# Kernel tuning notes

Hardware: AMD Instinct MI355X
Metric: run time of the kernel (lower is better)

The kernel has to match this reference:

```python
import jax, jax.numpy as jnp
import numpy as np

K, P, Q, D = 16, 1024, 1024, 64  # heads, value-in dim, out dim, head dim; P'=P, Q'=Q, D'=D
B, N = 2, 2048                   # batch, seq (self-attention: M=N)
TEMPERATURE = jnp.sqrt(jnp.float32(D))

def _xavier(key, shape):
    fan_in, fan_out = shape[-2], shape[-1]
    lim = jnp.sqrt(6.0 / (fan_in + fan_out))
    return jax.random.uniform(key, shape, jnp.float32, -lim, lim)

def setup_inputs() -> dict:
    key = jax.random.key(0)
    k0, k1, k2, k3, k4 = jax.random.split(key, 5)
    return {
        'y_prime': jax.random.normal(k0, (B, N, Q), jnp.float32),
        'mask': jnp.zeros((N, N), jnp.float32),  # log-domain additive mask [M,N]
        'Lam_x': _xavier(k1, (K, P, D)),  # Lambda^(x): [K,P',D']
        'Lam_y': _xavier(k2, (K, Q, D)),  # Lambda^(y): [K,Q',D']
        'Th_x': _xavier(k3, (K, P, D)),   # Theta^(x):  [K,P,D]
        'Th_y': _xavier(k4, (K, Q, D)),   # Theta^(y):  [K,Q,D]
    }

def reference(y_prime, mask, Lam_x, Lam_y, Th_x, Th_y):
    # self-attention: x' = x = y'
    x_p = y_prime
    x = x_p
    # key projection: [B,M,K,D']
    r = jnp.einsum('bmp,kpd->bmkd', x_p, Lam_x)
    # bilinear scores: [K,B,M,N]
    r = jnp.einsum('bmkd,kqd,bnq->kbmn', r, Lam_y, y_prime)
    r = r + mask[None, None, :, :]
    # softmax over M (axis=-2), scaled by sqrt(D')
    A = jax.nn.softmax(r / TEMPERATURE, axis=-2)
    # value aggregation: [B,N,K,D]
    r = jnp.einsum('kbmn,bmp,kpd->bnkd', A, x, Th_x)
    # output projection: [B,N,Q]
    return jnp.einsum('bnkd,kqd->bnq', r, Th_y)
```

## Files before the change

kernel.cpp:

```cpp
#include <hip/hip_runtime.h>
#include <hip/hip_bf16.h>

#define KH 16
#define PD 1024
#define QD 1024
#define DD 64
#define BB 2
#define NN 2048
#define BN 4096
#define ST 72
#define SOFT_C 12.0f

typedef unsigned short u16;
typedef __attribute__((ext_vector_type(8))) short bf16x8;
typedef __attribute__((ext_vector_type(4))) short bf16x4;
typedef __attribute__((ext_vector_type(4))) float f32x4;

__device__ __forceinline__ float bf2f(u16 u) {
    return __uint_as_float(((unsigned)u) << 16);
}
__device__ __forceinline__ u16 f2bf(float f) {
    unsigned x = __float_as_uint(f);
    x += 0x7FFFu + ((x >> 16) & 1u);
    return (u16)(x >> 16);
}
__device__ __forceinline__ f32x4 mfma_k32(bf16x8 a, bf16x8 b, f32x4 c) {
    return __builtin_amdgcn_mfma_f32_16x16x32_bf16(a, b, c, 0, 0, 0);
}
__device__ __forceinline__ f32x4 mfma_k16(bf16x4 a, bf16x4 b, f32x4 c) {
#if __has_builtin(__builtin_amdgcn_mfma_f32_16x16x16bf16_1k)
    return __builtin_amdgcn_mfma_f32_16x16x16bf16_1k(a, b, c, 0, 0, 0);
#else
    asm("v_mfma_f32_16x16x16_bf16 %0, %1, %2, %0" : "+v"(c) : "v"(a), "v"(b));
    return c;
#endif
}
__device__ __forceinline__ bf16x8 ldfrag(const u16* base, int r0, int kc, int lane) {
    return *reinterpret_cast<const bf16x8*>(base + (r0 + (lane & 15)) * ST + kc +
                                            ((lane >> 4) << 3));
}
__device__ __forceinline__ bf16x4 ldfrag4(const u16* base, int r0, int kc, int lane) {
    return *reinterpret_cast<const bf16x4*>(base + (r0 + (lane & 15)) * ST + kc +
                                            ((lane >> 4) << 2));
}
__device__ __forceinline__ bf16x8 ldfragL(const u16* base, int r0, int kc, int lane) {
    return *reinterpret_cast<const bf16x8*>(base + ((r0 + (lane & 15)) << 6) + kc +
                                            ((lane >> 4) << 3));
}
__device__ __forceinline__ bf16x4 pack4(float a, float b, float c, float d) {
    union { bf16x4 v; __hip_bfloat162 h[2]; } u;
    u.h[0] = __float22bfloat162_rn(make_float2(a, b));
    u.h[1] = __float22bfloat162_rn(make_float2(c, d));
    return u.v;
}
__device__ __forceinline__ void gl_lds16(const u16* g, u16* l) {
    __builtin_amdgcn_global_load_lds(
        (const __attribute__((address_space(1))) void*)g,
        (__attribute__((address_space(3))) void*)l, 16, 0, 0);
}
template <int ROWS>
__device__ __forceinline__ void stage_dma(const u16* __restrict__ src, int ld,
                                          u16* dst, int lane, int w) {
#pragma unroll
    for (int c = 0; c < ROWS / 32; ++c) {
        int rbase = (w * (ROWS / 32) + c) * 8;
        const u16* g = src + (size_t)(rbase + (lane >> 3)) * ld + ((lane & 7) << 3);
        gl_lds16(g, dst + (rbase << 6));
    }
}
template <int ROWS, int NT>
__device__ __forceinline__ void stage_rows(const u16* __restrict__ src, int ld,
                                           u16* dst, int tid) {
#pragma unroll
    for (int it = 0; it < ROWS * 8 / NT; ++it) {
        int chunk = it * NT + tid;
        int row = chunk >> 3, col = (chunk & 7) << 3;
        *reinterpret_cast<uint4*>(dst + row * ST + col) =
            *reinterpret_cast<const uint4*>(src + row * ld + col);
    }
}

__global__ void detect_kernel(const u16* __restrict__ y, int* flag, int* mnz) {
    __shared__ int cnt;
    if (threadIdx.x == 0) cnt = 0;
    __syncthreads();
    int local = 0;
    for (int i = threadIdx.x; i < 8192; i += 256) {
        u16 u = y[i];
        int e = (u >> 7) & 0xFF;
        if (u == 0 || (e >= 96 && e < 160)) local++;
    }
    atomicAdd(&cnt, local);
    __syncthreads();
    if (threadIdx.x == 0) {
        *flag = (cnt > 7372) ? 1 : 0;
        *mnz = 0;
    }
}

__global__ __launch_bounds__(256) void mcheck_kernel(const void* __restrict__ msrc,
                                                     const int* __restrict__ flag,
                                                     int* mnz) {
    size_t n4 = (size_t)NN * NN / 8;
    if (*flag == 0) n4 *= 2;
    const uint4* p = (const uint4*)msrc;
    unsigned acc = 0;
    for (size_t i = blockIdx.x * 256 + threadIdx.x; i < n4;
         i += (size_t)gridDim.x * 256) {
        uint4 v = p[i];
        acc |= v.x | v.y | v.z | v.w;
    }
    if (acc) atomicOr(mnz, 1);
}

__global__ __launch_bounds__(256) void convert_kernel(
    const void* __restrict__ src, u16* __restrict__ dst, int n,
    const int* __restrict__ flag) {
    int i = (blockIdx.x * 256 + threadIdx.x) * 4;
    if (i >= n) return;
    if (*flag) {
        *reinterpret_cast<uint2*>(dst + i) =
            *reinterpret_cast<const uint2*>((const u16*)src + i);
    } else {
        float4 f = *reinterpret_cast<const float4*>((const float*)src + i);
        u16 t[4] = {f2bf(f.x), f2bf(f.y), f2bf(f.z), f2bf(f.w)};
        *reinterpret_cast<uint2*>(dst + i) = *reinterpret_cast<uint2*>(t);
    }
}

__global__ __launch_bounds__(256) void maskc_kernel(const void* __restrict__ src,
                                                    u16* __restrict__ dst,
                                                    const int* __restrict__ flag,
                                                    const int* __restrict__ mnz) {
    if (*mnz == 0) return;
    size_t i = ((size_t)blockIdx.x * 256 + threadIdx.x) * 8;
    float f[8];
    if (*flag) {
        uint4 v = *reinterpret_cast<const uint4*>((const u16*)src + i);
        u16 t[8];
        *reinterpret_cast<uint4*>(t) = v;
#pragma unroll
        for (int e = 0; e < 8; ++e) f[e] = bf2f(t[e]);
    } else {
        float4 a = *reinterpret_cast<const float4*>((const float*)src + i);
        float4 b = *reinterpret_cast<const float4*>((const float*)src + i + 4);
        f[0] = a.x; f[1] = a.y; f[2] = a.z; f[3] = a.w;
        f[4] = b.x; f[5] = b.y; f[6] = b.z; f[7] = b.w;
    }
    u16 t[8];
#pragma unroll
    for (int e = 0; e < 8; ++e) t[e] = f2bf(f[e] * 0.125f);
    *reinterpret_cast<uint4*>(dst + i) = *reinterpret_cast<uint4*>(t);
}

__global__ __launch_bounds__(256) void prew_kernel(
    const void* __restrict__ s0, const void* __restrict__ s1,
    const void* __restrict__ s2, const void* __restrict__ s3,
    u16* __restrict__ LamXt, u16* __restrict__ LamYt, u16* __restrict__ ThXt,
    u16* __restrict__ ThYr, const int* __restrict__ flag) {
    int z = blockIdx.z, k = blockIdx.y, tid = threadIdx.x;
    int isbf = *flag;
    if (z < 3) {
        const void* src = (z == 0) ? s0 : (z == 1) ? s1 : s2;
        u16* dst = (z == 0) ? LamXt : (z == 1) ? LamYt : ThXt;
        float scale = (z == 1) ? 0.125f : 1.0f;
        int p0 = blockIdx.x * 64;
        __shared__ float T[64][65];
        const u16* s16 = (const u16*)src + ((size_t)k * PD + p0) * DD;
        const float* s32 = (const float*)src + ((size_t)k * PD + p0) * DD;
#pragma unroll
        for (int it = 0; it < 2; ++it) {
            int chunk = it * 256 + tid;
            int row = chunk >> 3, c8 = (chunk & 7) << 3;
            float f[8];
            if (isbf) {
                uint4 v = *reinterpret_cast<const uint4*>(s16 + row * DD + c8);
                u16 t[8];
                *reinterpret_cast<uint4*>(t) = v;
#pragma unroll
                for (int e = 0; e < 8; ++e) f[e] = bf2f(t[e]);
            } else {
                float4 a = *reinterpret_cast<const float4*>(s32 + row * DD + c8);
                float4 b = *reinterpret_cast<const float4*>(s32 + row * DD + c8 + 4);
                f[0] = a.x; f[1] = a.y; f[2] = a.z; f[3] = a.w;
                f[4] = b.x; f[5] = b.y; f[6] = b.z; f[7] = b.w;
            }
#pragma unroll
            for (int e = 0; e < 8; ++e) T[row][c8 + e] = f[e] * scale;
        }
        __syncthreads();
        u16* drow = dst + (size_t)k * DD * PD + p0;
#pragma unroll
        for (int it = 0; it < 2; ++it) {
            int chunk = it * 256 + tid;
            int d = chunk >> 3, c8 = (chunk & 7) << 3;
            u16 t[8];
#pragma unroll
            for (int e = 0; e < 8; ++e) t[e] = f2bf(T[c8 + e][d]);
            *reinterpret_cast<uint4*>(drow + (size_t)d * PD + c8) =
                *reinterpret_cast<uint4*>(t);
        }
    } else {
        int q0 = blockIdx.x * 64;
#pragma unroll
        for (int it = 0; it < 2; ++it) {
            int chunk = it * 256 + tid;
            int row = chunk >> 3, c8 = (chunk & 7) << 3;
            size_t si = ((size_t)k * QD + q0 + row) * DD + c8;
            u16 t[8];
            if (isbf) {
                *reinterpret_cast<uint4*>(t) =
                    *reinterpret_cast<const uint4*>((const u16*)s3 + si);
            } else {
                float4 a = *reinterpret_cast<const float4*>((const float*)s3 + si);
                float4 b = *reinterpret_cast<const float4*>((const float*)s3 + si + 4);
                t[0] = f2bf(a.x); t[1] = f2bf(a.y); t[2] = f2bf(a.z); t[3] = f2bf(a.w);
                t[4] = f2bf(b.x); t[5] = f2bf(b.y); t[6] = f2bf(b.z); t[7] = f2bf(b.w);
            }
            *reinterpret_cast<uint4*>(ThYr + (size_t)(q0 + row) * (KH * DD) +
                                      k * DD + c8) = *reinterpret_cast<uint4*>(t);
        }
    }
}

__global__ __launch_bounds__(256, 3) void proj_gemm(
    const u16* __restrict__ A,
    const u16* __restrict__ Bm,
    u16* __restrict__ Xk, u16* __restrict__ Yk, u16* __restrict__ Vtg) {
    int tid = threadIdx.x, lane = tid & 63, w = tid >> 6;
    int mhalf = w & 1, nhalf = w >> 1;
    int m0 = blockIdx.x * 128, n0 = blockIdx.y * 128;
    __shared__ u16 As[128 * 64];
    __shared__ u16 Bs[128 * 64];
    f32x4 acc[4][4] = {};

    for (int kk = 0; kk < PD; kk += 64) {
        __syncthreads();
        stage_dma<128>(A + (size_t)m0 * PD + kk, PD, As, lane, w);
        stage_dma<128>(Bm + (size_t)n0 * PD + kk, PD, Bs, lane, w);
        __syncthreads();
#pragma unroll
        for (int kc = 0; kc < 64; kc += 32) {
            bf16x8 af[4], bf[4];
#pragma unroll
            for (int i = 0; i < 4; ++i) af[i] = ldfragL(As, mhalf * 64 + i * 16, kc, lane);
#pragma unroll
            for (int j = 0; j < 4; ++j) bf[j] = ldfragL(Bs, nhalf * 64 + j * 16, kc, lane);
#pragma unroll
            for (int i = 0; i < 4; ++i)
#pragma unroll
                for (int j = 0; j < 4; ++j) acc[i][j] = mfma_k32(af[i], bf[j], acc[i][j]);
        }
    }
    int nsel = n0 + nhalf * 64;
    int s = nsel >> 10, kh = (nsel >> 6) & 15;
    int quad = lane >> 4, col = lane & 15;
    if (s == 2) {
        u16* vb = Vtg + (size_t)kh * DD * BN;
#pragma unroll
        for (int i = 0; i < 4; ++i)
#pragma unroll
            for (int j = 0; j < 4; ++j) {
                int d = j * 16 + col;
                int mrow = m0 + mhalf * 64 + i * 16 + quad * 4;
                *reinterpret_cast<bf16x4*>(vb + (size_t)d * BN + mrow) =
                    pack4(acc[i][j][0], acc[i][j][1], acc[i][j][2], acc[i][j][3]);
            }
    } else {
        u16* ob = (s == 0 ? Xk : Yk) + (size_t)kh * BN * DD;
#pragma unroll
        for (int i = 0; i < 4; ++i)
#pragma unroll
            for (int j = 0; j < 4; ++j)
#pragma unroll
                for (int reg = 0; reg < 4; ++reg) {
                    int mrow = m0 + mhalf * 64 + i * 16 + quad * 4 + reg;
                    ob[(size_t)mrow * DD + j * 16 + col] = f2bf(acc[i][j][reg]);
                }
    }
}

__global__ __launch_bounds__(256, 4) void attn_kernel(
    const u16* __restrict__ Xk,
    const u16* __restrict__ Yk,
    const u16* __restrict__ Vtg,
    const u16* __restrict__ maskc,
    const int* __restrict__ mnz,
    int mlen,
    u16* __restrict__ Op0,
    u16* __restrict__ Op1,
    float* __restrict__ lbuf) {
    int tid = threadIdx.x, lane = tid & 63, w = tid >> 6;
    int quad = lane >> 4, col = lane & 15;
    int q0 = blockIdx.x * 128, k = blockIdx.y;
    int z = blockIdx.z, b = z & 1, s = z >> 1;
    const u16* Qp = Yk + ((size_t)k * BN + b * NN + q0) * DD;
    const u16* Kp = Xk + ((size_t)k * BN + b * NN) * DD;
    const u16* Vp = Vtg + (size_t)k * DD * BN + b * NN;
    __shared__ u16 Qs[128 * ST];
    __shared__ u16 Ks[64 * ST];
    __shared__ u16 Vt[64 * ST];
    int mz = *mnz;

    stage_rows<128, 256>(Qp, DD, Qs, tid);
    __syncthreads();
    bf16x8 qf[2][2];
#pragma unroll
    for (int g = 0; g < 2; ++g)
#pragma unroll
        for (int kc = 0; kc < 2; ++kc)
            qf[g][kc] = ldfrag(Qs, w * 32 + g * 16, kc * 32, lane);

    float lp[2] = {0.0f, 0.0f};
    f32x4 oacc[2][4] = {};

    int mbeg = s * mlen;
    for (int m0 = mbeg; m0 < mbeg + mlen; m0 += 64) {
        __syncthreads();
        stage_rows<64, 256>(Kp + (size_t)m0 * DD, DD, Ks, tid);
        stage_rows<64, 256>(Vp + m0, BN, Vt, tid);
        __syncthreads();

        f32x4 sacc[2][4] = {};
#pragma unroll
        for (int kg = 0; kg < 4; ++kg) {
            bf16x8 a0 = ldfrag(Ks, kg * 16, 0, lane);
            bf16x8 a1 = ldfrag(Ks, kg * 16, 32, lane);
#pragma unroll
            for (int g = 0; g < 2; ++g) {
                sacc[g][kg] = mfma_k32(a0, qf[g][0], sacc[g][kg]);
                sacc[g][kg] = mfma_k32(a1, qf[g][1], sacc[g][kg]);
            }
        }
        if (mz) {
#pragma unroll
            for (int g = 0; g < 2; ++g)
#pragma unroll
                for (int kg = 0; kg < 4; ++kg)
#pragma unroll
                    for (int reg = 0; reg < 4; ++reg)
                        sacc[g][kg][reg] += bf2f(
                            maskc[(size_t)(m0 + kg * 16 + quad * 4 + reg) * NN +
                                  q0 + w * 32 + g * 16 + col]);
        }
        bf16x4 pb[2][4];
#pragma unroll
        for (int g = 0; g < 2; ++g)
#pragma unroll
            for (int kg = 0; kg < 4; ++kg) {
                float p0 = __expf(sacc[g][kg][0] - SOFT_C);
                float p1 = __expf(sacc[g][kg][1] - SOFT_C);
                float p2 = __expf(sacc[g][kg][2] - SOFT_C);
                float p3 = __expf(sacc[g][kg][3] - SOFT_C);
                lp[g] += (p0 + p1) + (p2 + p3);
                pb[g][kg] = pack4(p0, p1, p2, p3);
            }
#pragma unroll
        for (int kg = 0; kg < 4; ++kg)
#pragma unroll
            for (int dg = 0; dg < 4; ++dg) {
                bf16x4 av = ldfrag4(Vt, dg * 16, kg * 16, lane);
#pragma unroll
                for (int g = 0; g < 2; ++g)
                    oacc[g][dg] = mfma_k16(av, pb[g][kg], oacc[g][dg]);
            }
    }

    float inv[2], lfull[2];
#pragma unroll
    for (int g = 0; g < 2; ++g) {
        float l = lp[g];
        l += __shfl_xor(l, 16);
        l += __shfl_xor(l, 32);
        lfull[g] = l;
        inv[g] = 1.0f / l;
    }
    u16* Od = s ? Op1 : Op0;
    if (quad == 0) {
#pragma unroll
        for (int g = 0; g < 2; ++g)
            lbuf[(size_t)s * (BN * KH) +
                 (size_t)(b * NN + q0 + w * 32 + g * 16 + col) * KH + k] = lfull[g];
    }
#pragma unroll
    for (int g = 0; g < 2; ++g)
#pragma unroll
        for (int dg = 0; dg < 4; ++dg)
            *reinterpret_cast<bf16x4*>(Qs + (w * 32 + g * 16 + col) * ST + dg * 16 +
                                       quad * 4) =
                pack4(oacc[g][dg][0] * inv[g], oacc[g][dg][1] * inv[g],
                      oacc[g][dg][2] * inv[g], oacc[g][dg][3] * inv[g]);
    __syncthreads();
    int r = tid >> 1, h = tid & 1;
    const u16* srow = Qs + r * ST + h * 32;
    u16* drow = Od + (size_t)(b * NN + q0 + r) * (KH * DD) + k * DD + h * 32;
#pragma unroll
    for (int u = 0; u < 4; ++u)
        *reinterpret_cast<uint4*>(drow + u * 8) =
            *reinterpret_cast<const uint4*>(srow + u * 8);
}

__global__ __launch_bounds__(256) void comb_kernel(u16* __restrict__ Op0,
                                                   const u16* __restrict__ Op1,
                                                   const float* __restrict__ lbuf) {
    size_t idx = ((size_t)blockIdx.x * 256 + threadIdx.x) * 8;
    size_t row = idx >> 10;
    int k = (int)((idx >> 6) & 15);
    float l0 = lbuf[row * KH + k];
    float l1 = lbuf[(size_t)BN * KH + row * KH + k];
    float w0 = l0 / (l0 + l1), w1 = 1.0f - w0;
    uint4 v0 = *reinterpret_cast<const uint4*>(Op0 + idx);
    uint4 v1 = *reinterpret_cast<const uint4*>(Op1 + idx);
    u16 a[8], b[8], o[8];
    *reinterpret_cast<uint4*>(a) = v0;
    *reinterpret_cast<uint4*>(b) = v1;
#pragma unroll
    for (int e = 0; e < 8; ++e) o[e] = f2bf(w0 * bf2f(a[e]) + w1 * bf2f(b[e]));
    *reinterpret_cast<uint4*>(Op0 + idx) = *reinterpret_cast<uint4*>(o);
}

__global__ __launch_bounds__(256, 3) void out_gemm(
    const u16* __restrict__ A,
    const u16* __restrict__ Bm,
    const int* __restrict__ flag,
    void* __restrict__ outv) {
    int tid = threadIdx.x, lane = tid & 63, w = tid >> 6;
    int mhalf = w & 1, nhalf = w >> 1;
    int m0 = blockIdx.x * 128, n0 = blockIdx.y * 128;
    __shared__ u16 As[128 * 64];
    __shared__ u16 Bs[128 * 64];
    f32x4 acc[4][4] = {};

    for (int kk = 0; kk < KH * DD; kk += 64) {
        __syncthreads();
        stage_dma<128>(A + (size_t)m0 * (KH * DD) + kk, KH * DD, As, lane, w);
        stage_dma<128>(Bm + (size_t)n0 * (KH * DD) + kk, KH * DD, Bs, lane, w);
        __syncthreads();
#pragma unroll
        for (int kc = 0; kc < 64; kc += 32) {
            bf16x8 af[4], bf[4];
#pragma unroll
            for (int i = 0; i < 4; ++i) af[i] = ldfragL(As, mhalf * 64 + i * 16, kc, lane);
#pragma unroll
            for (int j = 0; j < 4; ++j) bf[j] = ldfragL(Bs, nhalf * 64 + j * 16, kc, lane);
#pragma unroll
            for (int i = 0; i < 4; ++i)
#pragma unroll
                for (int j = 0; j < 4; ++j) acc[i][j] = mfma_k32(af[i], bf[j], acc[i][j]);
        }
    }
    int isbf = *flag;
    int quad = lane >> 4, col = lane & 15;
#pragma unroll
    for (int i = 0; i < 4; ++i)
#pragma unroll
        for (int j = 0; j < 4; ++j)
#pragma unroll
            for (int reg = 0; reg < 4; ++reg) {
                size_t row = m0 + mhalf * 64 + i * 16 + quad * 4 + reg;
                int c = n0 + nhalf * 64 + j * 16 + col;
                if (isbf)
                    ((u16*)outv)[row * QD + c] = f2bf(acc[i][j][reg]);
                else
                    ((float*)outv)[row * QD + c] = acc[i][j][reg];
            }
}

extern "C" void kernel_launch(void* const* d_in, const int* in_sizes, int n_in,
                              void* d_out, int out_size, void* d_ws, size_t ws_size,
                              hipStream_t stream) {
    char* wsb = (char*)d_ws;
    int* flag = (int*)wsb;
    int* mnz = (int*)(wsb + 16);
    u16* ycan = (u16*)(wsb + 64);
    const size_t NYP = (size_t)BN * PD;
    const size_t NW = (size_t)KH * PD * DD;
    const size_t OSZ = (size_t)BN * KH * DD;
    u16* Wcat = ycan + NYP;
    u16* ThYr = Wcat + 3 * NW;
    u16* Xk = ThYr + NW;
    u16* Yk = Xk + OSZ;
    u16* Vtg = Yk + OSZ;
    u16* maskc = Vtg + OSZ;
    u16* Op1 = maskc + (size_t)NN * NN;
    float* lbuf = (float*)(Op1 + OSZ);
    u16* Ob = ycan;

    size_t need2 = (size_t)((char*)(lbuf + 2 * (size_t)BN * KH) - wsb);
    int nsplit = (ws_size >= need2) ? 2 : 1;

    detect_kernel<<<1, 256, 0, stream>>>((const u16*)d_in[0], flag, mnz);
    mcheck_kernel<<<256, 256, 0, stream>>>(d_in[1], flag, mnz);
    convert_kernel<<<(int)(NYP / 1024), 256, 0, stream>>>(d_in[0], ycan, (int)NYP, flag);
    prew_kernel<<<dim3(16, KH, 4), 256, 0, stream>>>(
        d_in[2], d_in[3], d_in[4], d_in[5], Wcat, Wcat + NW, Wcat + 2 * NW, ThYr, flag);
    maskc_kernel<<<2048, 256, 0, stream>>>(d_in[1], maskc, flag, mnz);

    proj_gemm<<<dim3(BN / 128, 3072 / 128), 256, 0, stream>>>(ycan, Wcat, Xk, Yk, Vtg);
    attn_kernel<<<dim3(NN / 128, KH, BB * nsplit), 256, 0, stream>>>(
        Xk, Yk, Vtg, maskc, mnz, NN / nsplit, Ob, Op1, lbuf);
    if (nsplit == 2)
        comb_kernel<<<(int)(OSZ / 8 / 256), 256, 0, stream>>>(Ob, Op1, lbuf);
    out_gemm<<<dim3(BN / 128, QD / 128), 256, 0, stream>>>(Ob, ThYr, flag, d_out);
}
```

Baseline: 244.9 us.

## Fuse prep kernels, stage projection epilogue via LDS, drop attention split

Merges the mask check, input conversion, weight transposes and mask conversion into a single multi-role prep kernel, so several small launches become one. The projection GEMM epilogue now goes through shared memory so global writes are coalesced 16-byte stores instead of scattered scalar or 4-wide stores. The two-way split over the key dimension in attention is removed along with the combine kernel, so there are no partial outputs or combine pass. In exchange, the mask is now always converted even when it is all zeros, and attention runs with half as many blocks.

```diff
diff --git a/kernel.cpp b/kernel.cpp
--- a/kernel.cpp
+++ b/kernel.cpp
@@ -98,73 +98,42 @@
     }
 }
 
-__global__ __launch_bounds__(256) void mcheck_kernel(const void* __restrict__ msrc,
-                                                     const int* __restrict__ flag,
-                                                     int* mnz) {
-    size_t n4 = (size_t)NN * NN / 8;
-    if (*flag == 0) n4 *= 2;
-    const uint4* p = (const uint4*)msrc;
-    unsigned acc = 0;
-    for (size_t i = blockIdx.x * 256 + threadIdx.x; i < n4;
-         i += (size_t)gridDim.x * 256) {
-        uint4 v = p[i];
-        acc |= v.x | v.y | v.z | v.w;
-    }
-    if (acc) atomicOr(mnz, 1);
-}
-
-__global__ __launch_bounds__(256) void convert_kernel(
-    const void* __restrict__ src, u16* __restrict__ dst, int n,
-    const int* __restrict__ flag) {
-    int i = (blockIdx.x * 256 + threadIdx.x) * 4;
-    if (i >= n) return;
-    if (*flag) {
-        *reinterpret_cast<uint2*>(dst + i) =
-            *reinterpret_cast<const uint2*>((const u16*)src + i);
-    } else {
-        float4 f = *reinterpret_cast<const float4*>((const float*)src + i);
-        u16 t[4] = {f2bf(f.x), f2bf(f.y), f2bf(f.z), f2bf(f.w)};
-        *reinterpret_cast<uint2*>(dst + i) = *reinterpret_cast<uint2*>(t);
-    }
-}
-
-__global__ __launch_bounds__(256) void maskc_kernel(const void* __restrict__ src,
-                                                    u16* __restrict__ dst,
-                                                    const int* __restrict__ flag,
-                                                    const int* __restrict__ mnz) {
-    if (*mnz == 0) return;
-    size_t i = ((size_t)blockIdx.x * 256 + threadIdx.x) * 8;
-    float f[8];
-    if (*flag) {
-        uint4 v = *reinterpret_cast<const uint4*>((const u16*)src + i);
-        u16 t[8];
-        *reinterpret_cast<uint4*>(t) = v;
-#pragma unroll
-        for (int e = 0; e < 8; ++e) f[e] = bf2f(t[e]);
-    } else {
-        float4 a = *reinterpret_cast<const float4*>((const float*)src + i);
-        float4 b = *reinterpret_cast<const float4*>((const float*)src + i + 4);
-        f[0] = a.x; f[1] = a.y; f[2] = a.z; f[3] = a.w;
-        f[4] = b.x; f[5] = b.y; f[6] = b.z; f[7] = b.w;
-    }
-    u16 t[8];
-#pragma unroll
-    for (int e = 0; e < 8; ++e) t[e] = f2bf(f[e] * 0.125f);
-    *reinterpret_cast<uint4*>(dst + i) = *reinterpret_cast<uint4*>(t);
-}
-
-__global__ __launch_bounds__(256) void prew_kernel(
+__global__ __launch_bounds__(256) void prep_kernel(
+    const void* __restrict__ ysrc, const void* __restrict__ msrc,
     const void* __restrict__ s0, const void* __restrict__ s1,
     const void* __restrict__ s2, const void* __restrict__ s3,
-    u16* __restrict__ LamXt, u16* __restrict__ LamYt, u16* __restrict__ ThXt,
-    u16* __restrict__ ThYr, const int* __restrict__ flag) {
-    int z = blockIdx.z, k = blockIdx.y, tid = threadIdx.x;
+    u16* __restrict__ ycan, u16* __restrict__ LamXt, u16* __restrict__ LamYt,
+    u16* __restrict__ ThXt, u16* __restrict__ ThYr, u16* __restrict__ maskc,
+    const int* __restrict__ flag, int* __restrict__ mnz) {
+    int z = blockIdx.z, bx = blockIdx.x, tid = threadIdx.x;
     int isbf = *flag;
-    if (z < 3) {
-        const void* src = (z == 0) ? s0 : (z == 1) ? s1 : s2;
-        u16* dst = (z == 0) ? LamXt : (z == 1) ? LamYt : ThXt;
-        float scale = (z == 1) ? 0.125f : 1.0f;
-        int p0 = blockIdx.x * 64;
+    if (z == 0) {
+        size_t n4 = (size_t)NN * NN / 8;
+        if (!isbf) n4 *= 2;
+        const uint4* p = (const uint4*)msrc;
+        unsigned acc = 0;
+        for (size_t i = (size_t)bx * 256 + tid; i < n4; i += 256 * 256) {
+            uint4 v = p[i];
+            acc |= v.x | v.y | v.z | v.w;
+        }
+        if (acc) atomicOr(mnz, 1);
+    } else if (z == 1) {
+        int n = BN * PD;
+        for (int i = (bx * 256 + tid) * 4; i < n; i += 256 * 256 * 4) {
+            if (isbf) {
+                *reinterpret_cast<uint2*>(ycan + i) =
+                    *reinterpret_cast<const uint2*>((const u16*)ysrc + i);
+            } else {
+                float4 f = *reinterpret_cast<const float4*>((const float*)ysrc + i);
+                u16 t[4] = {f2bf(f.x), f2bf(f.y), f2bf(f.z), f2bf(f.w)};
+                *reinterpret_cast<uint2*>(ycan + i) = *reinterpret_cast<uint2*>(t);
+            }
+        }
+    } else if (z <= 4) {
+        const void* src = (z == 2) ? s0 : (z == 3) ? s1 : s2;
+        u16* dst = (z == 2) ? LamXt : (z == 3) ? LamYt : ThXt;
+        float scale = (z == 3) ? 0.125f : 1.0f;
+        int k = bx >> 4, p0 = (bx & 15) * 64;
         __shared__ float T[64][65];
         const u16* s16 = (const u16*)src + ((size_t)k * PD + p0) * DD;
         const float* s32 = (const float*)src + ((size_t)k * PD + p0) * DD;
@@ -200,8 +169,8 @@
             *reinterpret_cast<uint4*>(drow + (size_t)d * PD + c8) =
                 *reinterpret_cast<uint4*>(t);
         }
-    } else {
-        int q0 = blockIdx.x * 64;
+    } else if (z == 5) {
+        int k = bx >> 4, q0 = (bx & 15) * 64;
 #pragma unroll
         for (int it = 0; it < 2; ++it) {
             int chunk = it * 256 + tid;
@@ -220,6 +189,28 @@
             *reinterpret_cast<uint4*>(ThYr + (size_t)(q0 + row) * (KH * DD) +
                                       k * DD + c8) = *reinterpret_cast<uint4*>(t);
         }
+    } else {
+        size_t n8 = (size_t)NN * NN / 8;
+        for (size_t c = (size_t)bx * 256 + tid; c < n8; c += 256 * 256) {
+            size_t i = c * 8;
+            float f[8];
+            if (isbf) {
+                uint4 v = *reinterpret_cast<const uint4*>((const u16*)msrc + i);
+                u16 t[8];
+                *reinterpret_cast<uint4*>(t) = v;
+#pragma unroll
+                for (int e = 0; e < 8; ++e) f[e] = bf2f(t[e]);
+            } else {
+                float4 a = *reinterpret_cast<const float4*>((const float*)msrc + i);
+                float4 b = *reinterpret_cast<const float4*>((const float*)msrc + i + 4);
+                f[0] = a.x; f[1] = a.y; f[2] = a.z; f[3] = a.w;
+                f[4] = b.x; f[5] = b.y; f[6] = b.z; f[7] = b.w;
+            }
+            u16 t[8];
+#pragma unroll
+            for (int e = 0; e < 8; ++e) t[e] = f2bf(f[e] * 0.125f);
+            *reinterpret_cast<uint4*>(maskc + i) = *reinterpret_cast<uint4*>(t);
+        }
     }
 }
 
@@ -252,31 +243,51 @@
                 for (int j = 0; j < 4; ++j) acc[i][j] = mfma_k32(af[i], bf[j], acc[i][j]);
         }
     }
-    int nsel = n0 + nhalf * 64;
-    int s = nsel >> 10, kh = (nsel >> 6) & 15;
+    int s = n0 >> 10;
     int quad = lane >> 4, col = lane & 15;
+    u16* stg = nhalf ? Bs : As;
+    __syncthreads();
     if (s == 2) {
-        u16* vb = Vtg + (size_t)kh * DD * BN;
 #pragma unroll
         for (int i = 0; i < 4; ++i)
 #pragma unroll
-            for (int j = 0; j < 4; ++j) {
-                int d = j * 16 + col;
-                int mrow = m0 + mhalf * 64 + i * 16 + quad * 4;
-                *reinterpret_cast<bf16x4*>(vb + (size_t)d * BN + mrow) =
+            for (int j = 0; j < 4; ++j)
+                *reinterpret_cast<bf16x4*>(stg + (j * 16 + col) * 128 + mhalf * 64 +
+                                           i * 16 + quad * 4) =
                     pack4(acc[i][j][0], acc[i][j][1], acc[i][j][2], acc[i][j][3]);
-            }
     } else {
-        u16* ob = (s == 0 ? Xk : Yk) + (size_t)kh * BN * DD;
 #pragma unroll
         for (int i = 0; i < 4; ++i)
 #pragma unroll
             for (int j = 0; j < 4; ++j)
 #pragma unroll
-                for (int reg = 0; reg < 4; ++reg) {
-                    int mrow = m0 + mhalf * 64 + i * 16 + quad * 4 + reg;
-                    ob[(size_t)mrow * DD + j * 16 + col] = f2bf(acc[i][j][reg]);
-                }
+                for (int reg = 0; reg < 4; ++reg)
+                    stg[(mhalf * 64 + i * 16 + quad * 4 + reg) * 64 + j * 16 + col] =
+                        f2bf(acc[i][j][reg]);
+    }
+    __syncthreads();
+#pragma unroll
+    for (int h = 0; h < 2; ++h) {
+        int kh = ((n0 + h * 64) >> 6) & 15;
+        const u16* src = h ? Bs : As;
+        if (s == 2) {
+            u16* vb = Vtg + (size_t)kh * DD * BN + m0;
+#pragma unroll
+            for (int it = 0; it < 4; ++it) {
+                int chunk = it * 256 + tid;
+                int d = chunk >> 4, off = (chunk & 15) * 8;
+                *reinterpret_cast<uint4*>(vb + (size_t)d * BN + off) =
+                    *reinterpret_cast<const uint4*>(src + d * 128 + off);
+            }
+        } else {
+            u16* ob = (s == 0 ? Xk : Yk) + (size_t)kh * BN * DD + (size_t)m0 * DD;
+#pragma unroll
+            for (int it = 0; it < 4; ++it) {
+                int chunk = it * 256 + tid;
+                *reinterpret_cast<uint4*>(ob + chunk * 8) =
+                    *reinterpret_cast<const uint4*>(src + chunk * 8);
+            }
+        }
     }
 }
 
@@ -286,14 +297,10 @@
     const u16* __restrict__ Vtg,
     const u16* __restrict__ maskc,
     const int* __restrict__ mnz,
-    int mlen,
-    u16* __restrict__ Op0,
-    u16* __restrict__ Op1,
-    float* __restrict__ lbuf) {
+    u16* __restrict__ O) {
     int tid = threadIdx.x, lane = tid & 63, w = tid >> 6;
     int quad = lane >> 4, col = lane & 15;
-    int q0 = blockIdx.x * 128, k = blockIdx.y;
-    int z = blockIdx.z, b = z & 1, s = z >> 1;
+    int q0 = blockIdx.x * 128, k = blockIdx.y, b = blockIdx.z;
     const u16* Qp = Yk + ((size_t)k * BN + b * NN + q0) * DD;
     const u16* Kp = Xk + ((size_t)k * BN + b * NN) * DD;
     const u16* Vp = Vtg + (size_t)k * DD * BN + b * NN;
@@ -314,8 +321,7 @@
     float lp[2] = {0.0f, 0.0f};
     f32x4 oacc[2][4] = {};
 
-    int mbeg = s * mlen;
-    for (int m0 = mbeg; m0 < mbeg + mlen; m0 += 64) {
+    for (int m0 = 0; m0 < NN; m0 += 64) {
         __syncthreads();
         stage_rows<64, 256>(Kp + (size_t)m0 * DD, DD, Ks, tid);
         stage_rows<64, 256>(Vp + m0, BN, Vt, tid);
@@ -366,21 +372,13 @@
             }
     }
 
-    float inv[2], lfull[2];
+    float inv[2];
 #pragma unroll
     for (int g = 0; g < 2; ++g) {
         float l = lp[g];
         l += __shfl_xor(l, 16);
         l += __shfl_xor(l, 32);
-        lfull[g] = l;
         inv[g] = 1.0f / l;
-    }
-    u16* Od = s ? Op1 : Op0;
-    if (quad == 0) {
-#pragma unroll
-        for (int g = 0; g < 2; ++g)
-            lbuf[(size_t)s * (BN * KH) +
-                 (size_t)(b * NN + q0 + w * 32 + g * 16 + col) * KH + k] = lfull[g];
     }
 #pragma unroll
     for (int g = 0; g < 2; ++g)
@@ -393,30 +391,11 @@
     __syncthreads();
     int r = tid >> 1, h = tid & 1;
     const u16* srow = Qs + r * ST + h * 32;
-    u16* drow = Od + (size_t)(b * NN + q0 + r) * (KH * DD) + k * DD + h * 32;
+    u16* drow = O + (size_t)(b * NN + q0 + r) * (KH * DD) + k * DD + h * 32;
 #pragma unroll
     for (int u = 0; u < 4; ++u)
         *reinterpret_cast<uint4*>(drow + u * 8) =
             *reinterpret_cast<const uint4*>(srow + u * 8);
-}
-
-__global__ __launch_bounds__(256) void comb_kernel(u16* __restrict__ Op0,
-                                                   const u16* __restrict__ Op1,
-                                                   const float* __restrict__ lbuf) {
-    size_t idx = ((size_t)blockIdx.x * 256 + threadIdx.x) * 8;
-    size_t row = idx >> 10;
-    int k = (int)((idx >> 6) & 15);
-    float l0 = lbuf[row * KH + k];
-    float l1 = lbuf[(size_t)BN * KH + row * KH + k];
-    float w0 = l0 / (l0 + l1), w1 = 1.0f - w0;
-    uint4 v0 = *reinterpret_cast<const uint4*>(Op0 + idx);
-    uint4 v1 = *reinterpret_cast<const uint4*>(Op1 + idx);
-    u16 a[8], b[8], o[8];
-    *reinterpret_cast<uint4*>(a) = v0;
-    *reinterpret_cast<uint4*>(b) = v1;
-#pragma unroll
-    for (int e = 0; e < 8; ++e) o[e] = f2bf(w0 * bf2f(a[e]) + w1 * bf2f(b[e]));
-    *reinterpret_cast<uint4*>(Op0 + idx) = *reinterpret_cast<uint4*>(o);
 }
 
 __global__ __launch_bounds__(256, 3) void out_gemm(
@@ -482,24 +461,14 @@
     u16* Yk = Xk + OSZ;
     u16* Vtg = Yk + OSZ;
     u16* maskc = Vtg + OSZ;
-    u16* Op1 = maskc + (size_t)NN * NN;
-    float* lbuf = (float*)(Op1 + OSZ);
     u16* Ob = ycan;
 
-    size_t need2 = (size_t)((char*)(lbuf + 2 * (size_t)BN * KH) - wsb);
-    int nsplit = (ws_size >= need2) ? 2 : 1;
-
     detect_kernel<<<1, 256, 0, stream>>>((const u16*)d_in[0], flag, mnz);
-    mcheck_kernel<<<256, 256, 0, stream>>>(d_in[1], flag, mnz);
-    convert_kernel<<<(int)(NYP / 1024), 256, 0, stream>>>(d_in[0], ycan, (int)NYP, flag);
-    prew_kernel<<<dim3(16, KH, 4), 256, 0, stream>>>(
-        d_in[2], d_in[3], d_in[4], d_in[5], Wcat, Wcat + NW, Wcat + 2 * NW, ThYr, flag);
-    maskc_kernel<<<2048, 256, 0, stream>>>(d_in[1], maskc, flag, mnz);
-
+    prep_kernel<<<dim3(256, 1, 7), 256, 0, stream>>>(
+        d_in[0], d_in[1], d_in[2], d_in[3], d_in[4], d_in[5], ycan, Wcat,
+        Wcat + NW, Wcat + 2 * NW, ThYr, maskc, flag, mnz);
     proj_gemm<<<dim3(BN / 128, 3072 / 128), 256, 0, stream>>>(ycan, Wcat, Xk, Yk, Vtg);
-    attn_kernel<<<dim3(NN / 128, KH, BB * nsplit), 256, 0, stream>>>(
-        Xk, Yk, Vtg, maskc, mnz, NN / nsplit, Ob, Op1, lbuf);
-    if (nsplit == 2)
-        comb_kernel<<<(int)(OSZ / 8 / 256), 256, 0, stream>>>(Ob, Op1, lbuf);
+    attn_kernel<<<dim3(NN / 128, KH, BB), 256, 0, stream>>>(Xk, Yk, Vtg, maskc,
+                                                            mnz, Ob);
     out_gemm<<<dim3(BN / 128, QD / 128), 256, 0, stream>>>(Ob, ThYr, flag, d_out);
 }
```

Result: no change. 242.0 us (-1.2%).
